# Kernel tuning notes

Hardware: AMD Instinct MI355X
Metric: run time of the kernel (lower is better)

The kernel has to match this reference:

```python
import jax, jax.numpy as jnp
import numpy as np

EMBED_DIM = 768
NUM_HEAD = 12
HEAD_DIM = 64
SCALE = 1.0 / np.sqrt(HEAD_DIM)


def setup_inputs() -> dict:
    key = jax.random.key(0)
    k1, k2, k3, k4 = jax.random.split(key, 4)
    B, T = 2, 2048
    x = jax.random.normal(k1, (B, T, EMBED_DIM), dtype=jnp.float32)
    # nn.Linear(embed_dim, 3*embed_dim, bias=True): weight [3E, E], bias [3E]
    w_qkv = jax.random.normal(k2, (3 * EMBED_DIM, EMBED_DIM), dtype=jnp.float32) * (1.0 / np.sqrt(EMBED_DIM))
    b_qkv = jax.random.normal(k3, (3 * EMBED_DIM,), dtype=jnp.float32) * 0.02
    # nn.Linear(embed_dim, embed_dim, bias=False): weight [E, E]
    w_final = jax.random.normal(k4, (EMBED_DIM, EMBED_DIM), dtype=jnp.float32) * (1.0 / np.sqrt(EMBED_DIM))
    return {"x": x, "w_qkv": w_qkv, "b_qkv": b_qkv, "w_final": w_final}


def reference(x, w_qkv, b_qkv, w_final):
    B, T, E = x.shape
    # qkv projection: x @ W^T + b  -> [B, T, 3E]
    qkv = jnp.einsum('bte,fe->btf', x, w_qkv) + b_qkv
    q, k, v = jnp.split(qkv, 3, axis=-1)

    def heads(t):  # [B, T, E] -> [B, H, T, D]
        return t.reshape(B, T, NUM_HEAD, HEAD_DIM).transpose(0, 2, 1, 3)

    q, k, v = heads(q), heads(k), heads(v)
    # scores [B, H, T, T]
    scores = jnp.einsum('bhtd,bhsd->bhts', q, k) * SCALE
    causal = jnp.tril(jnp.ones((T, T), dtype=bool))
    scores = jnp.where(causal, scores, -jnp.inf)
    attn = jax.nn.softmax(scores, axis=-1)  # dropout off (eval mode)
    out = jnp.einsum('bhts,bhsd->bhtd', attn, v)  # [B, H, T, D]
    out = out.transpose(0, 2, 1, 3).reshape(B, T, NUM_HEAD * HEAD_DIM)
    return jnp.einsum('bte,fe->btf', out, w_final)
```

## Files before the change

kernel.cpp:

```cpp
#include <hip/hip_runtime.h>
#include <cstdint>

typedef _Float16 f16x8 __attribute__((ext_vector_type(8)));
typedef _Float16 f16x4 __attribute__((ext_vector_type(4)));
typedef float    f32x4 __attribute__((ext_vector_type(4)));

static constexpr int TB = 2;
static constexpr int TT = 2048;
static constexpr int TE = 768;
static constexpr int TH = 12;
static constexpr int TD = 64;
static constexpr int TM = TB * TT;
static constexpr int TK = TE;
static constexpr int NQKV = 3 * TE;

#define SCALE_LOG2E 0.18033688011112042f

__device__ __forceinline__ void gload16(const void* g, void* lds) {
  __builtin_amdgcn_global_load_lds(
      (__attribute__((address_space(1))) void*)(uintptr_t)g,
      (__attribute__((address_space(3))) void*)(uint32_t)(uintptr_t)lds, 16, 0, 0);
}

__global__ void cvt3(const float* __restrict__ x, const float* __restrict__ wq,
                     const float* __restrict__ wf, _Float16* __restrict__ xh,
                     _Float16* __restrict__ wqh, _Float16* __restrict__ wfh) {
  const int NX = TM * TK / 4, NW = NQKV * TK / 4;
  int i = blockIdx.x * 256 + threadIdx.x;
  if (i < NX) {
    float4 v = ((const float4*)x)[i];
    f16x4 o = {(_Float16)v.x, (_Float16)v.y, (_Float16)v.z, (_Float16)v.w};
    *(f16x4*)&xh[(size_t)i * 4] = o;
  } else {
    const float4* src; _Float16* dst; int j;
    if (i < NX + NW) { src = (const float4*)wq; dst = wqh; j = i - NX; }
    else             { src = (const float4*)wf; dst = wfh; j = i - NX - NW; }
    float4 v = src[j];
    f16x4 o = {(_Float16)v.x, (_Float16)v.y, (_Float16)v.z, (_Float16)v.w};
    const int flat = j * 4;
    const int n = flat / TK, k = flat % TK;
    const size_t idx = ((size_t)(n >> 4) * 24 + (k >> 5)) * 512 +
                       ((k >> 3) & 3) * 128 + (n & 15) * 8 + (k & 7);
    *(f16x4*)&dst[idx] = o;
  }
}

template <int EPI, int NXT>
__global__ __launch_bounds__(512)
void gemm_nt(const _Float16* __restrict__ A, const _Float16* __restrict__ Bw,
             const float* __restrict__ bias,
             _Float16* __restrict__ qb, _Float16* __restrict__ kb,
             _Float16* __restrict__ vtb, float* __restrict__ outp) {
  __shared__ _Float16 As[2][128 * 64];
  const int tid = threadIdx.x;
  const int w = tid >> 6, lane = tid & 63;
  const int lr = lane & 15, lk = lane >> 4;

  const int id = blockIdx.x;
  const int xcd = id & 7, j = id >> 3;
  const int m0 = (xcd * 4 + j / NXT) * 128;
  const int n0 = (j % NXT) * 128;
  const int wr = w >> 2, wc = w & 3;

  f32x4 acc[4][2] = {};
  const char* Ab = (const char*)(A + (size_t)m0 * TK);
  const char* WB = (const char*)Bw;
  const int nb = (n0 >> 4) + wc * 2;
  constexpr int NS = TK / 64;

  auto loadB = [&](int ks, f16x8 (&bf)[2][2]) {
#pragma unroll
    for (int ni = 0; ni < 2; ++ni)
#pragma unroll
      for (int kc = 0; kc < 2; ++kc)
        bf[ni][kc] = *(const f16x8*)(WB +
                                     ((size_t)(nb + ni) * 24 + ks * 2 + kc) * 1024 +
                                     lane * 16);
  };
  auto stageA = [&](int ks, int buf) {
#pragma unroll
    for (int c = 0; c < 2; ++c) {
      int g = w * 2 + c;
      int o = g * 1024 + lane * 16;
      int row = o >> 7, ch = (o >> 4) & 7;
      gload16(Ab + (size_t)row * (TK * 2) + ks * 128 + ((ch ^ (row & 7)) << 4),
              (char*)As[buf] + g * 1024);
    }
  };
  auto step = [&](f16x8 (&bc)[2][2], f16x8 (&bn)[2][2], int buf, int ks) {
    if (ks + 1 < NS) {
      loadB(ks + 1, bn);
      stageA(ks + 1, buf ^ 1);
      asm volatile("s_waitcnt vmcnt(6)" ::: "memory");
    } else {
      asm volatile("s_waitcnt vmcnt(0)" ::: "memory");
    }
    __builtin_amdgcn_s_barrier();
#pragma unroll
    for (int kc = 0; kc < 2; ++kc) {
      f16x8 af[4];
#pragma unroll
      for (int mi = 0; mi < 4; ++mi) {
        int row = wr * 64 + mi * 16 + lr;
        af[mi] =
            *(const f16x8*)&As[buf][row * 64 + (((kc * 4 + lk) ^ (row & 7)) << 3)];
      }
#pragma unroll
      for (int mi = 0; mi < 4; ++mi)
#pragma unroll
        for (int ni = 0; ni < 2; ++ni)
          acc[mi][ni] = __builtin_amdgcn_mfma_f32_16x16x32_f16(af[mi], bc[ni][kc],
                                                               acc[mi][ni], 0, 0, 0);
    }
    __builtin_amdgcn_s_barrier();
  };

  f16x8 bA[2][2], bB[2][2];
  loadB(0, bA);
  stageA(0, 0);
  for (int kss = 0; kss < NS; kss += 2) {
    step(bA, bB, 0, kss);
    step(bB, bA, 1, kss + 1);
  }

#pragma unroll
  for (int mi = 0; mi < 4; ++mi) {
#pragma unroll
    for (int ni = 0; ni < 2; ++ni) {
      const int col = n0 + wc * 32 + ni * 16 + lr;
#pragma unroll
      for (int r = 0; r < 4; ++r) {
        const int row = m0 + wr * 64 + mi * 16 + lk * 4 + r;
        float v = acc[mi][ni][r];
        if (EPI == 0) {
          v += bias[col];
          const int which = (col >= 2 * TE) ? 2 : (col >= TE ? 1 : 0);
          const int e = col - which * TE;
          const int h = e >> 6, d = e & 63;
          const int b = row >> 11, t = row & (TT - 1);
          const size_t hb = (size_t)(b * TH + h);
          if (which == 0) {
            qb[(hb * TT + t) * TD + d] = (_Float16)(v * SCALE_LOG2E);
          } else if (which == 1) {
            kb[((((hb * 128 + (t >> 4)) * 8 + (d >> 3)) * 16 + (t & 15)) * 8) +
               (d & 7)] = (_Float16)v;
          } else {
            const int kc = (t >> 5) & 1, hi = (t >> 4) & 1;
            const int lkv = (t >> 2) & 3, m = t & 3;
            vtb[((((((hb * 32 + (t >> 6)) * 4 + (d >> 4)) * 2 + kc) * 4 + lkv) *
                      16 +
                  (d & 15)) *
                 8) +
                (hi * 4 + m)] = (_Float16)v;
          }
        } else {
          outp[(size_t)row * TE + col] = v;
        }
      }
    }
  }
}

__global__ __launch_bounds__(256)
void attn_kernel(const _Float16* __restrict__ qbuf, const _Float16* __restrict__ kbuf,
                 const _Float16* __restrict__ vtbuf, _Float16* __restrict__ ob) {
  const int tid = threadIdx.x, w = tid >> 6, lane = tid & 63;
  const int lr = lane & 15, lk = lane >> 4;

  const int id = blockIdx.x;
  const int bh = id % 24;
  const int qt = 31 - id / 24;
  const int t0 = qt * 64;
  const int nt = qt + 1, ntm1 = qt;

  const _Float16* q = qbuf + (size_t)bh * (TT * TD);
  const char* kbase =
      (const char*)(kbuf + (size_t)bh * (TT * TD)) + lk * 256 + lr * 16;
  const char* vbase =
      (const char*)(vtbuf + (size_t)bh * (TT * TD)) + lk * 256 + lr * 16;

  f16x8 qf[2];
#pragma unroll
  for (int kc = 0; kc < 2; ++kc)
    qf[kc] = *(const f16x8*)&q[(size_t)(t0 + w * 16 + lr) * TD + kc * 32 + lk * 8];

  f32x4 of[4] = {};
  float mrun = -1e30f, lrun = 0.f;

  f16x8 kfA[2][4], kfB[2][4], vf[2][4];

#pragma unroll
  for (int kc = 0; kc < 2; ++kc)
#pragma unroll
    for (int ni = 0; ni < 4; ++ni)
      kfA[kc][ni] = *(const f16x8*)(kbase + ni * 2048 + kc * 1024);
  {
    const char* k1 = kbase + (size_t)(nt > 1 ? 1 : 0) * 8192;
#pragma unroll
    for (int kc = 0; kc < 2; ++kc)
#pragma unroll
      for (int ni = 0; ni < 4; ++ni)
        kfB[kc][ni] = *(const f16x8*)(k1 + ni * 2048 + kc * 1024);
  }

  auto phase = [&](f16x8 (&kf)[2][4], int st) {
    const char* vt = vbase + (size_t)st * 8192;
#pragma unroll
    for (int kc = 0; kc < 2; ++kc)
#pragma unroll
      for (int nd = 0; nd < 4; ++nd)
        vf[kc][nd] = *(const f16x8*)(vt + nd * 2048 + kc * 1024);

    f32x4 sa[4] = {};
    __builtin_amdgcn_s_setprio(1);
#pragma unroll
    for (int kc = 0; kc < 2; ++kc)
#pragma unroll
      for (int ni = 0; ni < 4; ++ni)
        sa[ni] =
            __builtin_amdgcn_mfma_f32_16x16x32_f16(kf[kc][ni], qf[kc], sa[ni], 0, 0, 0);
    __builtin_amdgcn_s_setprio(0);

    {
      const int stp = (st + 2 <= ntm1) ? st + 2 : ntm1;
      const char* kt = kbase + (size_t)stp * 8192;
#pragma unroll
      for (int kc = 0; kc < 2; ++kc)
#pragma unroll
        for (int ni = 0; ni < 4; ++ni)
          kf[kc][ni] = *(const f16x8*)(kt + ni * 2048 + kc * 1024);
    }

    if (st == ntm1) {
      const int s0 = st * 64;
#pragma unroll
      for (int ni = 0; ni < 4; ++ni)
#pragma unroll
        for (int r = 0; r < 4; ++r)
          if (s0 + ni * 16 + lk * 4 + r > t0 + w * 16 + lr) sa[ni][r] = -1e30f;
    }

    float mx;
    {
      float m0_ = fmaxf(fmaxf(sa[0][0], sa[0][1]), fmaxf(sa[0][2], sa[0][3]));
      float m1_ = fmaxf(fmaxf(sa[1][0], sa[1][1]), fmaxf(sa[1][2], sa[1][3]));
      float m2_ = fmaxf(fmaxf(sa[2][0], sa[2][1]), fmaxf(sa[2][2], sa[2][3]));
      float m3_ = fmaxf(fmaxf(sa[3][0], sa[3][1]), fmaxf(sa[3][2], sa[3][3]));
      mx = fmaxf(fmaxf(m0_, m1_), fmaxf(m2_, m3_));
      mx = fmaxf(mx, __shfl_xor(mx, 16));
      mx = fmaxf(mx, __shfl_xor(mx, 32));
    }

    if (__any(mx > mrun + 8.0f)) {
      float mn = fmaxf(mrun, mx);
      float al = __builtin_amdgcn_exp2f(mrun - mn);
      mrun = mn;
      lrun *= al;
      float al4[4];
#pragma unroll
      for (int r = 0; r < 4; ++r) al4[r] = __shfl(al, lk * 4 + r);
#pragma unroll
      for (int nd = 0; nd < 4; ++nd)
#pragma unroll
        for (int r = 0; r < 4; ++r) of[nd][r] *= al4[r];
    }

    f16x8 pa[2];
    float rs;
    {
      float rn[4];
#pragma unroll
      for (int ni = 0; ni < 4; ++ni) {
        float p0 = __builtin_amdgcn_exp2f(sa[ni][0] - mrun);
        float p1 = __builtin_amdgcn_exp2f(sa[ni][1] - mrun);
        float p2 = __builtin_amdgcn_exp2f(sa[ni][2] - mrun);
        float p3 = __builtin_amdgcn_exp2f(sa[ni][3] - mrun);
        rn[ni] = (p0 + p1) + (p2 + p3);
        pa[ni >> 1][(ni & 1) * 4 + 0] = (_Float16)p0;
        pa[ni >> 1][(ni & 1) * 4 + 1] = (_Float16)p1;
        pa[ni >> 1][(ni & 1) * 4 + 2] = (_Float16)p2;
        pa[ni >> 1][(ni & 1) * 4 + 3] = (_Float16)p3;
      }
      rs = (rn[0] + rn[1]) + (rn[2] + rn[3]);
      rs += __shfl_xor(rs, 16);
      rs += __shfl_xor(rs, 32);
    }
    lrun += rs;

    __builtin_amdgcn_s_setprio(1);
#pragma unroll
    for (int kc = 0; kc < 2; ++kc)
#pragma unroll
      for (int nd = 0; nd < 4; ++nd)
        of[nd] =
            __builtin_amdgcn_mfma_f32_16x16x32_f16(pa[kc], vf[kc][nd], of[nd], 0, 0, 0);
    __builtin_amdgcn_s_setprio(0);
  };

  int st = 0;
  while (st + 1 < nt) {
    phase(kfA, st);
    phase(kfB, st + 1);
    st += 2;
  }
  if (st < nt) phase(kfA, st);

  float linv[4];
#pragma unroll
  for (int r = 0; r < 4; ++r) linv[r] = __shfl(lrun, lk * 4 + r);
  const int b = bh / TH, h = bh - b * TH;
#pragma unroll
  for (int nd = 0; nd < 4; ++nd) {
#pragma unroll
    for (int r = 0; r < 4; ++r) {
      int tg = t0 + w * 16 + lk * 4 + r;
      int d = nd * 16 + lr;
      ob[(size_t)(b * TT + tg) * TE + h * TD + d] = (_Float16)(of[nd][r] / linv[r]);
    }
  }
}

extern "C" void kernel_launch(void* const* d_in, const int* in_sizes, int n_in,
                              void* d_out, int out_size, void* d_ws, size_t ws_size,
                              hipStream_t stream) {
  const float* x    = (const float*)d_in[0];
  const float* wqkv = (const float*)d_in[1];
  const float* bqkv = (const float*)d_in[2];
  const float* wfin = (const float*)d_in[3];
  float* out = (float*)d_out;

  _Float16* xh  = (_Float16*)d_ws;
  _Float16* wqh = xh + (size_t)TM * TK;
  _Float16* wfh = wqh + (size_t)NQKV * TK;
  _Float16* qb  = wfh + (size_t)TE * TE;
  _Float16* kb  = qb + (size_t)TM * TE;
  _Float16* vtb = kb + (size_t)TM * TE;
  _Float16* ob  = vtb + (size_t)TM * TE;

  cvt3<<<5376, 256, 0, stream>>>(x, wqkv, wfin, xh, wqh, wfh);
  gemm_nt<0, NQKV / 128><<<(NQKV / 128) * (TM / 128), 512, 0, stream>>>(
      xh, wqh, bqkv, qb, kb, vtb, nullptr);
  attn_kernel<<<dim3(TT / 64 * TB * TH), 256, 0, stream>>>(qb, kb, vtb, ob);
  gemm_nt<1, TE / 128><<<(TE / 128) * (TM / 128), 512, 0, stream>>>(
      ob, wfh, nullptr, nullptr, nullptr, nullptr, out);
}
```

Before: 87.80 us.

## Triple-buffer GEMM K pipeline and shrink M tile to 64 rows

The projection GEMMs now use a 64-row M tile with 256 threads, where each wave covers a 32-column slice and all 64 rows, so twice as many blocks are launched. The K loop moves from double to triple buffering in LDS and registers. Loads are issued two steps ahead, right after a single barrier, which removes the second barrier per step. The goal is more blocks to fill the CUs and better latency hiding, at the cost of less A-tile reuse per block and a reliance on the vmcnt accounting being right for the new load distance.

After: 82.18 us. 1.07x faster.

```diff
diff --git a/kernel.cpp b/kernel.cpp
--- a/kernel.cpp
+++ b/kernel.cpp
@@ -45,22 +45,23 @@
   }
 }
 
-template <int EPI, int NXT>
-__global__ __launch_bounds__(512)
+template <int EPI, int MT, int NXT, int MPX>
+__global__ __launch_bounds__(MT * 4)
 void gemm_nt(const _Float16* __restrict__ A, const _Float16* __restrict__ Bw,
              const float* __restrict__ bias,
              _Float16* __restrict__ qb, _Float16* __restrict__ kb,
              _Float16* __restrict__ vtb, float* __restrict__ outp) {
-  __shared__ _Float16 As[2][128 * 64];
+  __shared__ _Float16 As[3][MT * 64];
   const int tid = threadIdx.x;
   const int w = tid >> 6, lane = tid & 63;
   const int lr = lane & 15, lk = lane >> 4;
 
   const int id = blockIdx.x;
   const int xcd = id & 7, j = id >> 3;
-  const int m0 = (xcd * 4 + j / NXT) * 128;
+  const int m0 = (xcd * MPX + j / NXT) * MT;
   const int n0 = (j % NXT) * 128;
-  const int wr = w >> 2, wc = w & 3;
+  const int wr = (MT == 128) ? (w >> 2) : 0;
+  const int wc = (MT == 128) ? (w & 3) : w;
 
   f32x4 acc[4][2] = {};
   const char* Ab = (const char*)(A + (size_t)m0 * TK);
@@ -77,33 +78,35 @@
                                      ((size_t)(nb + ni) * 24 + ks * 2 + kc) * 1024 +
                                      lane * 16);
   };
-  auto stageA = [&](int ks, int buf) {
+  auto stageA = [&](int ks, _Float16* L) {
 #pragma unroll
     for (int c = 0; c < 2; ++c) {
       int g = w * 2 + c;
       int o = g * 1024 + lane * 16;
       int row = o >> 7, ch = (o >> 4) & 7;
       gload16(Ab + (size_t)row * (TK * 2) + ks * 128 + ((ch ^ (row & 7)) << 4),
-              (char*)As[buf] + g * 1024);
+              (char*)L + g * 1024);
     }
   };
-  auto step = [&](f16x8 (&bc)[2][2], f16x8 (&bn)[2][2], int buf, int ks) {
-    if (ks + 1 < NS) {
-      loadB(ks + 1, bn);
-      stageA(ks + 1, buf ^ 1);
+  auto step = [&](f16x8 (&bc)[2][2], f16x8 (&bn)[2][2], _Float16* Lc,
+                  _Float16* Ln, int ks) {
+    if (ks < NS - 1) {
       asm volatile("s_waitcnt vmcnt(6)" ::: "memory");
     } else {
       asm volatile("s_waitcnt vmcnt(0)" ::: "memory");
     }
     __builtin_amdgcn_s_barrier();
+    if (ks < NS - 2) {
+      loadB(ks + 2, bn);
+      stageA(ks + 2, Ln);
+    }
 #pragma unroll
     for (int kc = 0; kc < 2; ++kc) {
       f16x8 af[4];
 #pragma unroll
       for (int mi = 0; mi < 4; ++mi) {
         int row = wr * 64 + mi * 16 + lr;
-        af[mi] =
-            *(const f16x8*)&As[buf][row * 64 + (((kc * 4 + lk) ^ (row & 7)) << 3)];
+        af[mi] = *(const f16x8*)&Lc[row * 64 + (((kc * 4 + lk) ^ (row & 7)) << 3)];
       }
 #pragma unroll
       for (int mi = 0; mi < 4; ++mi)
@@ -112,15 +115,17 @@
           acc[mi][ni] = __builtin_amdgcn_mfma_f32_16x16x32_f16(af[mi], bc[ni][kc],
                                                                acc[mi][ni], 0, 0, 0);
     }
-    __builtin_amdgcn_s_barrier();
   };
 
-  f16x8 bA[2][2], bB[2][2];
-  loadB(0, bA);
-  stageA(0, 0);
-  for (int kss = 0; kss < NS; kss += 2) {
-    step(bA, bB, 0, kss);
-    step(bB, bA, 1, kss + 1);
+  f16x8 b0[2][2], b1[2][2], b2[2][2];
+  loadB(0, b0);
+  stageA(0, As[0]);
+  loadB(1, b1);
+  stageA(1, As[1]);
+  for (int kss = 0; kss < NS; kss += 3) {
+    step(b0, b2, As[0], As[2], kss);
+    step(b1, b0, As[1], As[0], kss + 1);
+    step(b2, b1, As[2], As[1], kss + 2);
   }
 
 #pragma unroll
@@ -338,9 +343,9 @@
   _Float16* ob  = vtb + (size_t)TM * TE;
 
   cvt3<<<5376, 256, 0, stream>>>(x, wqkv, wfin, xh, wqh, wfh);
-  gemm_nt<0, NQKV / 128><<<(NQKV / 128) * (TM / 128), 512, 0, stream>>>(
+  gemm_nt<0, 64, NQKV / 128, 8><<<8 * 8 * (NQKV / 128), 256, 0, stream>>>(
       xh, wqh, bqkv, qb, kb, vtb, nullptr);
   attn_kernel<<<dim3(TT / 64 * TB * TH), 256, 0, stream>>>(qb, kb, vtb, ob);
-  gemm_nt<1, TE / 128><<<(TE / 128) * (TM / 128), 512, 0, stream>>>(
+  gemm_nt<1, 64, TE / 128, 8><<<8 * 8 * (TE / 128), 256, 0, stream>>>(
       ob, wfh, nullptr, nullptr, nullptr, nullptr, out);
 }
```
